# Performance work log

Hardware: AMD Instinct MI355X
Metric: run time of the kernel (lower is better)

## Reference

```python
import jax, jax.numpy as jnp
import numpy as np

DN = jax.lax.conv_dimension_numbers((1, 32, 32, 32, 1), (3, 3, 3, 1, 32), ('NDHWC', 'DHWIO', 'NDHWC'))


def setup_inputs() -> dict:
    key = jax.random.key(0)
    k0, k1, k2, k3, k4 = jax.random.split(key, 5)
    B = 64
    x = jax.random.normal(k0, (B, 32, 32, 32, 1), dtype=jnp.float32)
    # conv weights in DHWIO layout; kaiming-ish scale
    w1 = jax.random.normal(k1, (3, 3, 3, 1, 32), dtype=jnp.float32) * (1.0 / np.sqrt(27 * 1))
    b1 = jax.random.normal(k2, (32,), dtype=jnp.float32) * 0.01
    w2 = jax.random.normal(k3, (3, 3, 3, 32, 64), dtype=jnp.float32) * (1.0 / np.sqrt(27 * 32))
    b2 = jax.random.normal(k4, (64,), dtype=jnp.float32) * 0.01
    return {"x": x, "w1": w1, "b1": b1, "w2": w2, "b2": b2}


def _conv3d_valid(x, w):
    # x: [B, D, H, W, C_in], w: [kD, kH, kW, C_in, C_out] -> [B, D-2, H-2, W-2, C_out]
    dn = jax.lax.conv_dimension_numbers(x.shape, w.shape, ('NDHWC', 'DHWIO', 'NDHWC'))
    return jax.lax.conv_general_dilated(x, w, window_strides=(1, 1, 1),
                                        padding='VALID', dimension_numbers=dn)


def reference(x, w1, b1, w2, b2):
    # Dense input -> all voxels active, so spconv's gather-GEMM-scatter equals
    # a dense valid 3D conv. ReLU acts on active-site features == dense ReLU.
    h = jax.nn.relu(_conv3d_valid(x, w1) + b1)        # [B, 30, 30, 30, 32]
    h = jax.nn.relu(_conv3d_valid(h, w2) + b2)        # [B, 28, 28, 28, 64]
    # spconv ToDense returns NCDHW
    return jnp.transpose(h, (0, 4, 1, 2, 3))          # [B, 64, 28, 28, 28]
```

## Files before the change

### kernel.cpp

```cpp
#include <hip/hip_runtime.h>
#include <cstdint>
#include <cstddef>

typedef __attribute__((ext_vector_type(8))) short bf16x8;
typedef __attribute__((ext_vector_type(4))) float f32x4;
typedef __attribute__((ext_vector_type(4))) unsigned int u32x4;
typedef unsigned short u16;

#define H1_ROW_B   1920
#define H1_BATCH   (30 * 30 * 960)
#define LDS_STRIDE 1952
#define OUT_CSTR   21952

__device__ __forceinline__ u16 f2bf(float f) {
    union { float f; unsigned u; } v; v.f = f;
    unsigned r = v.u + 0x7FFF + ((v.u >> 16) & 1);
    return (u16)(r >> 16);
}

__device__ __forceinline__ void fma4(float4& a, float s, const float4& w) {
    a.x = fmaf(s, w.x, a.x);
    a.y = fmaf(s, w.y, a.y);
    a.z = fmaf(s, w.z, a.z);
    a.w = fmaf(s, w.w, a.w);
}

__device__ __forceinline__ void gld_lds(const char* src, unsigned char* dst) {
    __builtin_amdgcn_global_load_lds(
        (const __attribute__((address_space(1))) void*)src,
        (__attribute__((address_space(3))) void*)dst, 16, 0, 0);
}

__global__ __launch_bounds__(256) void conv1_relu(
    const float* __restrict__ x, const float* __restrict__ w1,
    const float* __restrict__ b1, u16* __restrict__ h1, int b0)
{
    __shared__ float wl[27 * 32 + 32];

    const int z   = blockIdx.x;
    const int yt  = blockIdx.y;
    const int bl  = blockIdx.z;
    const int b   = b0 + bl;
    const int tid = threadIdx.x;

    for (int i = tid; i < 27 * 32; i += 256) wl[i] = w1[i];
    if (tid < 32) wl[27 * 32 + tid] = b1[tid];
    __syncthreads();

    const int c4   = tid & 7;
    const int slot = tid >> 3;

    const float4 bias = *reinterpret_cast<const float4*>(&wl[27 * 32 + c4 * 4]);
    const float* xb  = x + (size_t)b * 32768;
    u16*         h1b = h1 + (size_t)bl * H1_BATCH;

    if (slot < 30) {
#pragma unroll 1
        for (int j = 0; j < 3; ++j) {
            const int p  = slot + 30 * j;
            const int yy = p / 15;
            const int xx = (p - yy * 15) * 2;
            const int y  = yt * 6 + yy;

            float4 acc0 = bias, acc1 = bias;
#pragma unroll
            for (int kd = 0; kd < 3; ++kd) {
#pragma unroll
                for (int kh = 0; kh < 3; ++kh) {
                    const float* row = xb + ((size_t)(z + kd) * 32 + (y + kh)) * 32 + xx;
                    const float2 v01 = *reinterpret_cast<const float2*>(row);
                    const float2 v23 = *reinterpret_cast<const float2*>(row + 2);
                    const int t = (kd * 3 + kh) * 3;
                    const float4 w0  = *reinterpret_cast<const float4*>(&wl[(t + 0) * 32 + c4 * 4]);
                    const float4 w1v = *reinterpret_cast<const float4*>(&wl[(t + 1) * 32 + c4 * 4]);
                    const float4 w2v = *reinterpret_cast<const float4*>(&wl[(t + 2) * 32 + c4 * 4]);
                    fma4(acc0, v01.x, w0);
                    fma4(acc0, v01.y, w1v);
                    fma4(acc0, v23.x, w2v);
                    fma4(acc1, v01.y, w0);
                    fma4(acc1, v23.x, w1v);
                    fma4(acc1, v23.y, w2v);
                }
            }
            ushort4 s0, s1;
            s0.x = f2bf(fmaxf(acc0.x, 0.f)); s0.y = f2bf(fmaxf(acc0.y, 0.f));
            s0.z = f2bf(fmaxf(acc0.z, 0.f)); s0.w = f2bf(fmaxf(acc0.w, 0.f));
            s1.x = f2bf(fmaxf(acc1.x, 0.f)); s1.y = f2bf(fmaxf(acc1.y, 0.f));
            s1.z = f2bf(fmaxf(acc1.z, 0.f)); s1.w = f2bf(fmaxf(acc1.w, 0.f));
            u16* dst = h1b + ((size_t)(z * 30 + y) * 30 + xx) * 32 + c4 * 4;
            *reinterpret_cast<ushort4*>(dst)      = s0;
            *reinterpret_cast<ushort4*>(dst + 32) = s1;
        }
    }
}

__global__ __launch_bounds__(256) void pack_w2(
    const float* __restrict__ w2, u16* __restrict__ wB)
{
    const int tap = blockIdx.x;
    const int tid = threadIdx.x;
    const int nt = tid >> 6;
    const int l  = tid & 63;
    const int r = l & 15, q = l >> 4;
    u16* dst = wB + ((size_t)(tap * 4 + nt) * 64 + l) * 8;
#pragma unroll
    for (int j = 0; j < 8; ++j)
        dst[j] = f2bf(w2[(size_t)(tap * 32 + q * 8 + j) * 64 + nt * 16 + r]);
}

__global__ __launch_bounds__(512, 4) void conv2_mfma(
    const u16* __restrict__ h1, const u16* __restrict__ wB,
    const float* __restrict__ b2, float* __restrict__ out, int b0)
{
    __shared__ __align__(16) unsigned char smem[36 * LDS_STRIDE];

    const int g   = gridDim.x;
    const int bid = blockIdx.x;
    const int lb  = (g % 8 == 0) ? ((bid & 7) * (g >> 3) + (bid >> 3)) : bid;

    const int t0  = lb % 49;
    const int bl  = lb / 49;
    const int yg  = t0 % 7;
    const int zt  = t0 / 7;

    const int b  = b0 + bl;
    const int y0 = yg * 4, z0 = zt * 4;
    const int tid = threadIdx.x;
    const int wv  = tid >> 6;
    const int l   = tid & 63;
    const int zw  = wv >> 1;
    const int nh  = wv & 1;
    const int r = l & 15, q = l >> 4;
    const int yl = r >> 2, xg = r & 3;

    const char* wBl = (const char*)wB + nh * 2048 + l * 16;

    {
        const char* gbase = (const char*)(h1 + (size_t)bl * H1_BATCH);
        for (int c = wv; c < 72; c += 8) {
            const int rid = c >> 1, half = c & 1;
            const int zz = rid / 6, yy = rid - zz * 6;
            const char* src = gbase
                + (size_t)((z0 + zz) * 30 + (y0 + yy)) * H1_ROW_B
                + half * 896 + l * 16;
            unsigned char* dst = smem + rid * LDS_STRIDE + half * 896 + l * 16;
            gld_lds(src, dst);
        }
    }
    __syncthreads();

    f32x4 acc[7][2];
    {
        const float bv0 = b2[nh * 32 + r];
        const float bv1 = b2[nh * 32 + 16 + r];
#pragma unroll
        for (int mt = 0; mt < 7; ++mt) {
            acc[mt][0] = (f32x4){bv0, bv0, bv0, bv0};
            acc[mt][1] = (f32x4){bv1, bv1, bv1, bv1};
        }
    }

    const unsigned char* aBase =
        smem + (zw * 6 + yl) * LDS_STRIDE + xg * 64 + q * 16;

    u32x4 Bs[3][2];
#define B_LOAD(slot, t)                                                        \
    { const char* p_ = wBl + (size_t)(t) * 4096;                               \
      asm volatile("global_load_dwordx4 %0, %2, off\n\t"                       \
                   "global_load_dwordx4 %1, %2, off offset:1024"               \
                   : "=&v"(Bs[slot][0]), "=&v"(Bs[slot][1]) : "v"(p_)); }

    B_LOAD(0, 0)
    B_LOAD(1, 1)

#pragma unroll
    for (int tap = 0; tap < 27; ++tap) {
        const int cur = tap % 3;

        if (tap < 25) B_LOAD((tap + 2) % 3, tap + 2)

        if (tap < 25)       asm volatile("s_waitcnt vmcnt(4)");
        else if (tap == 25) asm volatile("s_waitcnt vmcnt(2)");
        else                asm volatile("s_waitcnt vmcnt(0)");

        asm volatile("" : "+v"(Bs[cur][0]), "+v"(Bs[cur][1]));
        const bf16x8 B0 = __builtin_bit_cast(bf16x8, Bs[cur][0]);
        const bf16x8 B1 = __builtin_bit_cast(bf16x8, Bs[cur][1]);

        const int kd = tap / 9;
        const int kh = (tap - kd * 9) / 3;
        const int kw = tap - kd * 9 - kh * 3;
        const unsigned char* ap = aBase + (kd * 6 + kh) * LDS_STRIDE + kw * 64;

#pragma unroll
        for (int mt = 0; mt < 7; ++mt) {
            const bf16x8 a = *reinterpret_cast<const bf16x8*>(ap + mt * 256);
            acc[mt][0] = __builtin_amdgcn_mfma_f32_16x16x32_bf16(a, B0, acc[mt][0], 0, 0, 0);
            acc[mt][1] = __builtin_amdgcn_mfma_f32_16x16x32_bf16(a, B1, acc[mt][1], 0, 0, 0);
        }
    }
#undef B_LOAD

    const int z = z0 + zw;
    float* ob = out + ((size_t)b * 64 + nh * 32 + r) * OUT_CSTR
                    + (size_t)z * 784 + (size_t)(y0 + q) * 28;
#pragma unroll
    for (int mt = 0; mt < 7; ++mt) {
#pragma unroll
        for (int nt = 0; nt < 2; ++nt) {
            const f32x4 v = acc[mt][nt];
            float4 st;
            st.x = fmaxf(v.x, 0.f);
            st.y = fmaxf(v.y, 0.f);
            st.z = fmaxf(v.z, 0.f);
            st.w = fmaxf(v.w, 0.f);
            *reinterpret_cast<float4*>(ob + (size_t)nt * 16 * OUT_CSTR + mt * 4) = st;
        }
    }
}

extern "C" void kernel_launch(void* const* d_in, const int* in_sizes, int n_in,
                              void* d_out, int out_size, void* d_ws, size_t ws_size,
                              hipStream_t stream)
{
    const float* x  = (const float*)d_in[0];
    const float* w1 = (const float*)d_in[1];
    const float* b1 = (const float*)d_in[2];
    const float* w2 = (const float*)d_in[3];
    const float* b2 = (const float*)d_in[4];
    float* out = (float*)d_out;

    u16* wB = (u16*)d_ws;
    u16* h1 = (u16*)((char*)d_ws + 131072);

    pack_w2<<<27, 256, 0, stream>>>(w2, wB);

    const size_t per_batch = (size_t)H1_BATCH * 2;
    size_t avail = ws_size > 131072 ? ws_size - 131072 : 0;
    int bchunk = (int)(avail / per_batch);
    if (bchunk < 1)  bchunk = 1;
    if (bchunk > 64) bchunk = 64;

    for (int b0 = 0; b0 < 64; b0 += bchunk) {
        int bc = 64 - b0;
        if (bc > bchunk) bc = bchunk;
        conv1_relu<<<dim3(30, 5, bc), 256, 0, stream>>>(x, w1, b1, h1, b0);
        conv2_mfma<<<dim3(49 * bc), 512, 0, stream>>>(h1, wB, b2, out, b0);
    }
}
```

Before: 272.0 us.

## Fuse conv1 into conv2 kernel, recomputing h1 halo tiles in LDS

Removes the separate conv1 kernel and its h1 buffer in global memory. Each conv2 block now loads its 6x8x32 input patch, rounds it to bf16, computes conv1+ReLU for the 6x6 h1 rows it needs directly into LDS, and then runs the MFMA conv2. This removes the h1 write and read round trip through HBM and the batch-chunk launch loop. In exchange, conv1 work on halo rows is repeated across neighbouring blocks, LDS use grows, and the input is now rounded to bf16 before conv1, which slightly changes numerics.

```diff
diff --git a/kernel.cpp b/kernel.cpp
--- a/kernel.cpp
+++ b/kernel.cpp
@@ -7,15 +7,21 @@
 typedef __attribute__((ext_vector_type(4))) unsigned int u32x4;
 typedef unsigned short u16;
 
-#define H1_ROW_B   1920
-#define H1_BATCH   (30 * 30 * 960)
 #define LDS_STRIDE 1952
+#define XBUF_OFF   (36 * LDS_STRIDE)
+#define WL_OFF     (XBUF_OFF + 4096)
+#define SMEM_BYTES (WL_OFF + 3584)
 #define OUT_CSTR   21952
 
 __device__ __forceinline__ u16 f2bf(float f) {
     union { float f; unsigned u; } v; v.f = f;
     unsigned r = v.u + 0x7FFF + ((v.u >> 16) & 1);
     return (u16)(r >> 16);
+}
+
+__device__ __forceinline__ float bf2f(u16 u) {
+    union { unsigned u; float f; } v; v.u = ((unsigned)u) << 16;
+    return v.f;
 }
 
 __device__ __forceinline__ void fma4(float4& a, float s, const float4& w) {
@@ -23,75 +29,6 @@
     a.y = fmaf(s, w.y, a.y);
     a.z = fmaf(s, w.z, a.z);
     a.w = fmaf(s, w.w, a.w);
-}
-
-__device__ __forceinline__ void gld_lds(const char* src, unsigned char* dst) {
-    __builtin_amdgcn_global_load_lds(
-        (const __attribute__((address_space(1))) void*)src,
-        (__attribute__((address_space(3))) void*)dst, 16, 0, 0);
-}
-
-__global__ __launch_bounds__(256) void conv1_relu(
-    const float* __restrict__ x, const float* __restrict__ w1,
-    const float* __restrict__ b1, u16* __restrict__ h1, int b0)
-{
-    __shared__ float wl[27 * 32 + 32];
-
-    const int z   = blockIdx.x;
-    const int yt  = blockIdx.y;
-    const int bl  = blockIdx.z;
-    const int b   = b0 + bl;
-    const int tid = threadIdx.x;
-
-    for (int i = tid; i < 27 * 32; i += 256) wl[i] = w1[i];
-    if (tid < 32) wl[27 * 32 + tid] = b1[tid];
-    __syncthreads();
-
-    const int c4   = tid & 7;
-    const int slot = tid >> 3;
-
-    const float4 bias = *reinterpret_cast<const float4*>(&wl[27 * 32 + c4 * 4]);
-    const float* xb  = x + (size_t)b * 32768;
-    u16*         h1b = h1 + (size_t)bl * H1_BATCH;
-
-    if (slot < 30) {
-#pragma unroll 1
-        for (int j = 0; j < 3; ++j) {
-            const int p  = slot + 30 * j;
-            const int yy = p / 15;
-            const int xx = (p - yy * 15) * 2;
-            const int y  = yt * 6 + yy;
-
-            float4 acc0 = bias, acc1 = bias;
-#pragma unroll
-            for (int kd = 0; kd < 3; ++kd) {
-#pragma unroll
-                for (int kh = 0; kh < 3; ++kh) {
-                    const float* row = xb + ((size_t)(z + kd) * 32 + (y + kh)) * 32 + xx;
-                    const float2 v01 = *reinterpret_cast<const float2*>(row);
-                    const float2 v23 = *reinterpret_cast<const float2*>(row + 2);
-                    const int t = (kd * 3 + kh) * 3;
-                    const float4 w0  = *reinterpret_cast<const float4*>(&wl[(t + 0) * 32 + c4 * 4]);
-                    const float4 w1v = *reinterpret_cast<const float4*>(&wl[(t + 1) * 32 + c4 * 4]);
-                    const float4 w2v = *reinterpret_cast<const float4*>(&wl[(t + 2) * 32 + c4 * 4]);
-                    fma4(acc0, v01.x, w0);
-                    fma4(acc0, v01.y, w1v);
-                    fma4(acc0, v23.x, w2v);
-                    fma4(acc1, v01.y, w0);
-                    fma4(acc1, v23.x, w1v);
-                    fma4(acc1, v23.y, w2v);
-                }
-            }
-            ushort4 s0, s1;
-            s0.x = f2bf(fmaxf(acc0.x, 0.f)); s0.y = f2bf(fmaxf(acc0.y, 0.f));
-            s0.z = f2bf(fmaxf(acc0.z, 0.f)); s0.w = f2bf(fmaxf(acc0.w, 0.f));
-            s1.x = f2bf(fmaxf(acc1.x, 0.f)); s1.y = f2bf(fmaxf(acc1.y, 0.f));
-            s1.z = f2bf(fmaxf(acc1.z, 0.f)); s1.w = f2bf(fmaxf(acc1.w, 0.f));
-            u16* dst = h1b + ((size_t)(z * 30 + y) * 30 + xx) * 32 + c4 * 4;
-            *reinterpret_cast<ushort4*>(dst)      = s0;
-            *reinterpret_cast<ushort4*>(dst + 32) = s1;
-        }
-    }
 }
 
 __global__ __launch_bounds__(256) void pack_w2(
@@ -108,22 +45,22 @@
         dst[j] = f2bf(w2[(size_t)(tap * 32 + q * 8 + j) * 64 + nt * 16 + r]);
 }
 
-__global__ __launch_bounds__(512, 4) void conv2_mfma(
-    const u16* __restrict__ h1, const u16* __restrict__ wB,
-    const float* __restrict__ b2, float* __restrict__ out, int b0)
+__global__ __launch_bounds__(512, 4) void conv2_fused(
+    const float* __restrict__ x, const float* __restrict__ w1,
+    const float* __restrict__ b1, const u16* __restrict__ wB,
+    const float* __restrict__ b2, float* __restrict__ out)
 {
-    __shared__ __align__(16) unsigned char smem[36 * LDS_STRIDE];
+    __shared__ __align__(16) unsigned char smem[SMEM_BYTES];
 
     const int g   = gridDim.x;
     const int bid = blockIdx.x;
     const int lb  = (g % 8 == 0) ? ((bid & 7) * (g >> 3) + (bid >> 3)) : bid;
 
     const int t0  = lb % 49;
-    const int bl  = lb / 49;
+    const int b   = lb / 49;
     const int yg  = t0 % 7;
     const int zt  = t0 / 7;
 
-    const int b  = b0 + bl;
     const int y0 = yg * 4, z0 = zt * 4;
     const int tid = threadIdx.x;
     const int wv  = tid >> 6;
@@ -133,18 +70,73 @@
     const int r = l & 15, q = l >> 4;
     const int yl = r >> 2, xg = r & 3;
 
-    const char* wBl = (const char*)wB + nh * 2048 + l * 16;
-
     {
-        const char* gbase = (const char*)(h1 + (size_t)bl * H1_BATCH);
-        for (int c = wv; c < 72; c += 8) {
-            const int rid = c >> 1, half = c & 1;
-            const int zz = rid / 6, yy = rid - zz * 6;
-            const char* src = gbase
-                + (size_t)((z0 + zz) * 30 + (y0 + yy)) * H1_ROW_B
-                + half * 896 + l * 16;
-            unsigned char* dst = smem + rid * LDS_STRIDE + half * 896 + l * 16;
-            gld_lds(src, dst);
+        const float* xb = x + (size_t)b * 32768;
+        const int yy  = l >> 3;
+        const int xx4 = (l & 7) * 4;
+        const float4 v = *reinterpret_cast<const float4*>(
+            xb + ((size_t)(z0 + wv) * 32 + (y0 + yy)) * 32 + xx4);
+        ushort4 s;
+        s.x = f2bf(v.x); s.y = f2bf(v.y); s.z = f2bf(v.z); s.w = f2bf(v.w);
+        *reinterpret_cast<ushort4*>(
+            smem + XBUF_OFF + ((wv * 8 + yy) * 32 + xx4) * 2) = s;
+    }
+    if (tid < 224) {
+        const int idx = tid * 4;
+        float4 v;
+        if (idx < 864) v = *reinterpret_cast<const float4*>(w1 + idx);
+        else           v = *reinterpret_cast<const float4*>(b1 + (idx - 864));
+        *reinterpret_cast<float4*>(smem + WL_OFF + idx * 4) = v;
+    }
+    __syncthreads();
+
+    {
+        const float* wl = reinterpret_cast<const float*>(smem + WL_OFF);
+        const u16* xbuf = reinterpret_cast<const u16*>(smem + XBUF_OFF);
+#pragma unroll
+        for (int i = 0; i < 9; ++i) {
+            const int unit = tid + i * 512;
+            if (unit < 4320) {
+                const int row = unit / 120;
+                const int rem = unit - row * 120;
+                const int p   = rem >> 3;
+                const int c4  = rem & 7;
+                const int xx  = p * 2;
+                const int rz  = row / 6;
+                const int ry  = row - rz * 6;
+
+                const float4 bias = *reinterpret_cast<const float4*>(
+                    &wl[27 * 32 + c4 * 4]);
+                float4 acc0 = bias, acc1 = bias;
+#pragma unroll
+                for (int kd = 0; kd < 3; ++kd) {
+#pragma unroll
+                    for (int kh = 0; kh < 3; ++kh) {
+                        const ushort4 xr = *reinterpret_cast<const ushort4*>(
+                            &xbuf[((rz + kd) * 8 + (ry + kh)) * 32 + xx]);
+                        const float a0 = bf2f(xr.x), a1 = bf2f(xr.y);
+                        const float a2 = bf2f(xr.z), a3 = bf2f(xr.w);
+                        const int t = (kd * 3 + kh) * 3;
+                        const float4 w0  = *reinterpret_cast<const float4*>(&wl[(t + 0) * 32 + c4 * 4]);
+                        const float4 w1v = *reinterpret_cast<const float4*>(&wl[(t + 1) * 32 + c4 * 4]);
+                        const float4 w2v = *reinterpret_cast<const float4*>(&wl[(t + 2) * 32 + c4 * 4]);
+                        fma4(acc0, a0, w0);
+                        fma4(acc0, a1, w1v);
+                        fma4(acc0, a2, w2v);
+                        fma4(acc1, a1, w0);
+                        fma4(acc1, a2, w1v);
+                        fma4(acc1, a3, w2v);
+                    }
+                }
+                ushort4 s0, s1;
+                s0.x = f2bf(fmaxf(acc0.x, 0.f)); s0.y = f2bf(fmaxf(acc0.y, 0.f));
+                s0.z = f2bf(fmaxf(acc0.z, 0.f)); s0.w = f2bf(fmaxf(acc0.w, 0.f));
+                s1.x = f2bf(fmaxf(acc1.x, 0.f)); s1.y = f2bf(fmaxf(acc1.y, 0.f));
+                s1.z = f2bf(fmaxf(acc1.z, 0.f)); s1.w = f2bf(fmaxf(acc1.w, 0.f));
+                unsigned char* dst = smem + row * LDS_STRIDE + xx * 64 + c4 * 8;
+                *reinterpret_cast<ushort4*>(dst)      = s0;
+                *reinterpret_cast<ushort4*>(dst + 64) = s1;
+            }
         }
     }
     __syncthreads();
@@ -162,6 +154,7 @@
 
     const unsigned char* aBase =
         smem + (zw * 6 + yl) * LDS_STRIDE + xg * 64 + q * 16;
+    const char* wBl = (const char*)wB + nh * 2048 + l * 16;
 
     u32x4 Bs[3][2];
 #define B_LOAD(slot, t)                                                        \
@@ -231,20 +224,7 @@
     float* out = (float*)d_out;
 
     u16* wB = (u16*)d_ws;
-    u16* h1 = (u16*)((char*)d_ws + 131072);
 
     pack_w2<<<27, 256, 0, stream>>>(w2, wB);
-
-    const size_t per_batch = (size_t)H1_BATCH * 2;
-    size_t avail = ws_size > 131072 ? ws_size - 131072 : 0;
-    int bchunk = (int)(avail / per_batch);
-    if (bchunk < 1)  bchunk = 1;
-    if (bchunk > 64) bchunk = 64;
-
-    for (int b0 = 0; b0 < 64; b0 += bchunk) {
-        int bc = 64 - b0;
-        if (bc > bchunk) bc = bchunk;
-        conv1_relu<<<dim3(30, 5, bc), 256, 0, stream>>>(x, w1, b1, h1, b0);
-        conv2_mfma<<<dim3(49 * bc), 512, 0, stream>>>(h1, wB, b2, out, b0);
-    }
-}
+    conv2_fused<<<dim3(3136), 512, 0, stream>>>(x, w1, b1, wB, b2, out);
+}
```

Result: slower. 355.2 us (+30.6%).
